# Performance work log

Hardware: AMD Instinct MI355X
Metric: run time of the kernel (lower is better)

The kernel has to match this reference:

```python
import jax, jax.numpy as jnp
import numpy as np

N, E = 65536, 524288
IN_DIM, HID_DIM, OUT_DIM = 1024, 512, 256


def setup_inputs() -> dict:
    key = jax.random.key(0)
    k1, k2, k3, k4, k5, k6 = jax.random.split(key, 6)
    h = jax.random.normal(k1, (N, IN_DIM), dtype=jnp.float32)
    src = jax.random.randint(k2, (E,), 0, N, dtype=jnp.int64)
    dst = jax.random.randint(k3, (E,), 0, N, dtype=jnp.int64)
    # Glorot-uniform weights as in DGL GraphConv
    lim1 = float(np.sqrt(6.0 / (IN_DIM + HID_DIM)))
    lim2 = float(np.sqrt(6.0 / (HID_DIM + OUT_DIM)))
    W1 = jax.random.uniform(k4, (IN_DIM, HID_DIM), jnp.float32, -lim1, lim1)
    W2 = jax.random.uniform(k5, (HID_DIM, OUT_DIM), jnp.float32, -lim2, lim2)
    b1 = jnp.zeros((HID_DIM,), jnp.float32)
    b2 = jnp.zeros((OUT_DIM,), jnp.float32)
    return {"h": h, "W1": W1, "b1": b1, "W2": W2, "b2": b2, "src": src, "dst": dst}


def _graph_conv(x, W, b, src, dst, inv_sqrt_dout, inv_sqrt_din):
    # DGL GraphConv, norm='both': D_in^{-1/2} A D_out^{-1/2} X W + b
    # Apply dense transform first (in_dim >= out_dim path in DGL) -- same math.
    x = x * inv_sqrt_dout[:, None]
    x = x @ W  # [N, out]
    agg = jax.ops.segment_sum(x[src], dst, num_segments=x.shape[0])  # scatter-add over edges
    return agg * inv_sqrt_din[:, None] + b


def reference(h, W1, b1, W2, b2, src, dst):
    n = h.shape[0]
    ones = jnp.ones((src.shape[0],), h.dtype)
    deg_out = jnp.maximum(jax.ops.segment_sum(ones, src, num_segments=n), 1.0)
    deg_in = jnp.maximum(jax.ops.segment_sum(ones, dst, num_segments=n), 1.0)
    inv_sqrt_dout = jax.lax.rsqrt(deg_out)
    inv_sqrt_din = jax.lax.rsqrt(deg_in)
    x = _graph_conv(h, W1, b1, src, dst, inv_sqrt_dout, inv_sqrt_din)
    x = jax.nn.elu(x)  # act; dropout p=0 -> identity
    out = _graph_conv(x, W2, b2, src, dst, inv_sqrt_dout, inv_sqrt_din)
    return out  # last_act = Identity
```

## Files before the change

### kernel.cpp

```cpp
#include <hip/hip_runtime.h>
#include <hip/hip_bf16.h>

#define IN_DIM 1024
#define HID 512
#define OUTD 256

typedef __attribute__((ext_vector_type(8))) short short8;
typedef __attribute__((ext_vector_type(4))) float f32x4;
typedef __attribute__((ext_vector_type(8))) unsigned short ushort8e;
typedef __attribute__((ext_vector_type(4))) unsigned short ushort4e;

template<int F> struct VecSel;
template<> struct VecSel<8> { using T = ushort8e; };
template<> struct VecSel<4> { using T = ushort4e; };


__device__ inline unsigned short f2bf(float f) {
    union { float f; unsigned u; } v; v.f = f;
    unsigned r = (v.u + 0x7FFF + ((v.u >> 16) & 1)) >> 16;
    return (unsigned short)r;
}

__device__ inline float bf2f(unsigned short u) {
    union { unsigned u; float f; } v; v.u = ((unsigned)u) << 16; return v.f;
}

__device__ inline void gload16(const void* g, void* l) {
    __builtin_amdgcn_global_load_lds(
        (const __attribute__((address_space(1))) void*)g,
        (__attribute__((address_space(3))) void*)l, 16, 0, 0);
}


__global__ void deg_kernel(const int* __restrict__ src, const int* __restrict__ dst,
                           int* __restrict__ dego, int* __restrict__ degi, int E) {
    int i = blockIdx.x * blockDim.x + threadIdx.x;
    if (i < E) {
        atomicAdd(&dego[src[i]], 1);
        atomicAdd(&degi[dst[i]], 1);
    }
}

__global__ void invsqrt_kernel(const int* __restrict__ dego, const int* __restrict__ degi,
                               float* __restrict__ iso, float* __restrict__ isi, int n) {
    int i = blockIdx.x * blockDim.x + threadIdx.x;
    if (i < n) {
        iso[i] = rsqrtf(fmaxf((float)dego[i], 1.0f));
        isi[i] = rsqrtf(fmaxf((float)degi[i], 1.0f));
    }
}


__global__ __launch_bounds__(256) void scan_block(const int* __restrict__ deg,
                                                  int* __restrict__ excl,
                                                  int* __restrict__ partials) {
    __shared__ int tmp[256];
    int tid = threadIdx.x;
    int i = blockIdx.x * 256 + tid;
    int v = deg[i];
    tmp[tid] = v;
    __syncthreads();
    #pragma unroll
    for (int off = 1; off < 256; off <<= 1) {
        int t = (tid >= off) ? tmp[tid - off] : 0;
        __syncthreads();
        tmp[tid] += t;
        __syncthreads();
    }
    excl[i] = tmp[tid] - v;
    if (tid == 255) partials[blockIdx.x] = tmp[255];
}

__global__ __launch_bounds__(256) void scan_partials(int* __restrict__ partials) {
    __shared__ int tmp[256];
    int tid = threadIdx.x;
    int v = partials[tid];
    tmp[tid] = v;
    __syncthreads();
    #pragma unroll
    for (int off = 1; off < 256; off <<= 1) {
        int t = (tid >= off) ? tmp[tid - off] : 0;
        __syncthreads();
        tmp[tid] += t;
        __syncthreads();
    }
    partials[tid] = tmp[tid] - v;
}

__global__ __launch_bounds__(256) void scan_add(const int* __restrict__ excl,
                                                const int* __restrict__ partials,
                                                const int* __restrict__ deg,
                                                int* __restrict__ row_start,
                                                int* __restrict__ cursor, int n) {
    int i = blockIdx.x * 256 + threadIdx.x;
    int v = excl[i] + partials[blockIdx.x];
    row_start[i] = v;
    cursor[i] = v;
    if (i == n - 1) row_start[n] = v + deg[i];
}

__global__ void csr_fill(const int* __restrict__ src, const int* __restrict__ dst,
                         int* __restrict__ cursor, int* __restrict__ eidx, int E) {
    int e = blockIdx.x * blockDim.x + threadIdx.x;
    if (e < E) {
        int pos = atomicAdd(&cursor[dst[e]], 1);
        eidx[pos] = src[e];
    }
}


__global__ void transpose_cvt(const float* __restrict__ W, unsigned short* __restrict__ Wt,
                              int K, int N) {
    int i = blockIdx.x * 256 + threadIdx.x;
    if (i < N * K) {
        int n = i / K, k = i - n * K;
        Wt[i] = f2bf(W[(size_t)k * N + n]);
    }
}


#define TM 128
#define TN 128
#define TK 32
#define NXCD 8

template<int AF32>
__global__ __launch_bounds__(256) void gemm_bf16_mfma(
    const void* __restrict__ Ap, const unsigned short* __restrict__ Bt,
    const float* __restrict__ rowscale, unsigned short* __restrict__ Cb,
    int M, int K, int Nc)
{
    __shared__ unsigned short As[TM][TK];
    __shared__ unsigned short Bs[TN][TK];

    const int tid  = threadIdx.x;
    const int lane = tid & 63;
    const int wave = tid >> 6;
    const int wr = wave >> 1, wc = wave & 1;
    const int lrow = lane & 15;
    const int lkg  = lane >> 4;

    const int nwg = gridDim.x;
    const int per = nwg / NXCD;
    const int lin = blockIdx.x;
    const int newlin = (lin % NXCD) * per + lin / NXCD;
    const int ncb = Nc / TN;
    const int m0 = (newlin / ncb) * TM;
    const int n0 = (newlin % ncb) * TN;

    const int s0 = wave * 64 + lane;
    const int s1 = s0 + 256;
    const int r0 = s0 >> 2, q0 = (s0 & 3) ^ ((s0 >> 3) & 3);
    const int r1 = s1 >> 2, q1 = (s1 & 3) ^ ((s1 >> 3) & 3);

    char* AsB = (char*)&As[0][0];
    char* BsB = (char*)&Bs[0][0];
    void* ldsA0 = AsB + wave * 1024;
    void* ldsA1 = AsB + 4096 + wave * 1024;
    void* ldsB0 = BsB + wave * 1024;
    void* ldsB1 = BsB + 4096 + wave * 1024;

    const int rA = tid >> 2;
    const int g  = tid & 3;
    const int jA = g ^ ((rA >> 1) & 3);
    float sc0 = 1.f, sc1 = 1.f;
    if (AF32) {
        sc0 = rowscale[m0 + rA];
        sc1 = rowscale[m0 + rA + 64];
    }
    const float* Af = (const float*)Ap;
    const unsigned short* Ab = (const unsigned short*)Ap;

    const int rslot = (lkg ^ ((lrow >> 1) & 3)) * 8;

    f32x4 acc[4][4] = {};

    const int nk = K / TK;
    for (int kt = 0; kt < nk; ++kt) {
        const int k0 = kt * TK;

        gload16(Bt + (size_t)(n0 + r0) * K + k0 + q0 * 8, ldsB0);
        gload16(Bt + (size_t)(n0 + r1) * K + k0 + q1 * 8, ldsB1);

        if (AF32) {
            const float* pa0 = Af + (size_t)(m0 + rA) * K + k0 + g * 8;
            const float* pa1 = Af + (size_t)(m0 + rA + 64) * K + k0 + g * 8;
            float4 u0 = *reinterpret_cast<const float4*>(pa0);
            float4 u1 = *reinterpret_cast<const float4*>(pa0 + 4);
            float4 w0 = *reinterpret_cast<const float4*>(pa1);
            float4 w1 = *reinterpret_cast<const float4*>(pa1 + 4);
            short8 pk0, pk1;
            pk0[0] = (short)f2bf(u0.x * sc0); pk0[1] = (short)f2bf(u0.y * sc0);
            pk0[2] = (short)f2bf(u0.z * sc0); pk0[3] = (short)f2bf(u0.w * sc0);
            pk0[4] = (short)f2bf(u1.x * sc0); pk0[5] = (short)f2bf(u1.y * sc0);
            pk0[6] = (short)f2bf(u1.z * sc0); pk0[7] = (short)f2bf(u1.w * sc0);
            pk1[0] = (short)f2bf(w0.x * sc1); pk1[1] = (short)f2bf(w0.y * sc1);
            pk1[2] = (short)f2bf(w0.z * sc1); pk1[3] = (short)f2bf(w0.w * sc1);
            pk1[4] = (short)f2bf(w1.x * sc1); pk1[5] = (short)f2bf(w1.y * sc1);
            pk1[6] = (short)f2bf(w1.z * sc1); pk1[7] = (short)f2bf(w1.w * sc1);
            *reinterpret_cast<short8*>(AsB + rA * 64 + jA * 16) = pk0;
            *reinterpret_cast<short8*>(AsB + (rA + 64) * 64 + jA * 16) = pk1;
        } else {
            gload16(Ab + (size_t)(m0 + r0) * K + k0 + q0 * 8, ldsA0);
            gload16(Ab + (size_t)(m0 + r1) * K + k0 + q1 * 8, ldsA1);
        }
        __syncthreads();

        short8 af[4], bfr[4];
        #pragma unroll
        for (int mi = 0; mi < 4; ++mi)
            af[mi] = *reinterpret_cast<const short8*>(&As[wr * 64 + mi * 16 + lrow][rslot]);
        #pragma unroll
        for (int ni = 0; ni < 4; ++ni)
            bfr[ni] = *reinterpret_cast<const short8*>(&Bs[wc * 64 + ni * 16 + lrow][rslot]);

        #pragma unroll
        for (int mi = 0; mi < 4; ++mi)
            #pragma unroll
            for (int ni = 0; ni < 4; ++ni)
                acc[mi][ni] = __builtin_amdgcn_mfma_f32_16x16x32_bf16(
                    af[mi], bfr[ni], acc[mi][ni], 0, 0, 0);

        __syncthreads();
    }

    #pragma unroll
    for (int mi = 0; mi < 4; ++mi)
        #pragma unroll
        for (int ni = 0; ni < 4; ++ni)
            #pragma unroll
            for (int r = 0; r < 4; ++r)
                Cb[(size_t)(m0 + wr * 64 + mi * 16 + lkg * 4 + r) * Nc
                   + (n0 + wc * 64 + ni * 16 + lrow)] = f2bf(acc[mi][ni][r]);
}


template<int DIM, bool LAYER1>
__global__ __launch_bounds__(256) void aggregate(
    const int* __restrict__ row_start, const int* __restrict__ eidx,
    const unsigned short* __restrict__ Xb, const float* __restrict__ isi,
    const float* __restrict__ iso, const float* __restrict__ bias,
    unsigned short* __restrict__ out_bf, float* __restrict__ out_f)
{
    constexpr int F = DIM / 64;
    using VecT = typename VecSel<F>::T;
    const int node = blockIdx.x * 4 + (threadIdx.x >> 6);
    const int lane = threadIdx.x & 63;

    const int beg = row_start[node];
    const int end = row_start[node + 1];
    const unsigned short* base = Xb + lane * F;

    float acc[F] = {};
    int e = beg;
    for (; e + 1 < end; e += 2) {
        int i0 = eidx[e], i1 = eidx[e + 1];
        VecT v0 = *reinterpret_cast<const VecT*>(base + (size_t)i0 * DIM);
        VecT v1 = *reinterpret_cast<const VecT*>(base + (size_t)i1 * DIM);
        #pragma unroll
        for (int f = 0; f < F; ++f) { acc[f] += bf2f(v0[f]); acc[f] += bf2f(v1[f]); }
    }
    if (e < end) {
        VecT v0 = *reinterpret_cast<const VecT*>(base + (size_t)eidx[e] * DIM);
        #pragma unroll
        for (int f = 0; f < F; ++f) acc[f] += bf2f(v0[f]);
    }

    const float si = isi[node];
    float bv[F];
    #pragma unroll
    for (int q = 0; q < F / 4; ++q)
        *reinterpret_cast<float4*>(&bv[q * 4]) =
            *reinterpret_cast<const float4*>(bias + lane * F + q * 4);

    if (LAYER1) {
        const float so = iso[node];
        short8 o;
        #pragma unroll
        for (int f = 0; f < F; ++f) {
            float v = acc[f] * si + bv[f];
            v = v > 0.f ? v : expm1f(v);
            o[f] = (short)f2bf(v * so);
        }
        *reinterpret_cast<short8*>(out_bf + (size_t)node * DIM + lane * F) = o;
    } else {
        #pragma unroll
        for (int q = 0; q < F / 4; ++q) {
            float4 v = make_float4(acc[q * 4 + 0] * si + bv[q * 4 + 0],
                                   acc[q * 4 + 1] * si + bv[q * 4 + 1],
                                   acc[q * 4 + 2] * si + bv[q * 4 + 2],
                                   acc[q * 4 + 3] * si + bv[q * 4 + 3]);
            *reinterpret_cast<float4*>(out_f + (size_t)node * DIM + lane * F + q * 4) = v;
        }
    }
}


extern "C" void kernel_launch(void* const* d_in, const int* in_sizes, int n_in,
                              void* d_out, int out_size, void* d_ws, size_t ws_size,
                              hipStream_t stream) {
    const float* h  = (const float*)d_in[0];
    const float* W1 = (const float*)d_in[1];
    const float* b1 = (const float*)d_in[2];
    const float* W2 = (const float*)d_in[3];
    const float* b2 = (const float*)d_in[4];
    const int*   src = (const int*)d_in[5];
    const int*   dst = (const int*)d_in[6];

    const int N = in_sizes[0] / IN_DIM;
    const int E = in_sizes[5];
    float* out = (float*)d_out;

    int* dego      = (int*)d_ws;
    int* degi      = dego + N;
    int* excl      = degi + N;
    int* partials  = excl + N;
    int* row_start = partials + 256;
    int* cursor    = row_start + N + 64;
    int* eidx      = cursor + N;
    float* iso     = (float*)(eidx + E);
    float* isi     = iso + N;
    unsigned short* W1t = (unsigned short*)(isi + N);
    unsigned short* W2t = W1t + (size_t)IN_DIM * HID;
    unsigned short* X1b = W2t + (size_t)HID * OUTD;
    unsigned short* X2b = X1b;
    unsigned short* R2h = X1b + (size_t)N * HID;

    hipMemsetAsync(dego, 0, sizeof(int) * (size_t)2 * N, stream);

    deg_kernel<<<(E + 255) / 256, 256, 0, stream>>>(src, dst, dego, degi, E);
    invsqrt_kernel<<<(N + 255) / 256, 256, 0, stream>>>(dego, degi, iso, isi, N);

    scan_block<<<N / 256, 256, 0, stream>>>(degi, excl, partials);
    scan_partials<<<1, 256, 0, stream>>>(partials);
    scan_add<<<N / 256, 256, 0, stream>>>(excl, partials, degi, row_start, cursor, N);
    csr_fill<<<(E + 255) / 256, 256, 0, stream>>>(src, dst, cursor, eidx, E);

    transpose_cvt<<<(IN_DIM * HID + 255) / 256, 256, 0, stream>>>(W1, W1t, IN_DIM, HID);
    transpose_cvt<<<(HID * OUTD + 255) / 256, 256, 0, stream>>>(W2, W2t, HID, OUTD);

    gemm_bf16_mfma<1><<<(N / TM) * (HID / TN), 256, 0, stream>>>(
        h, W1t, iso, X1b, N, IN_DIM, HID);
    aggregate<HID, true><<<N / 4, 256, 0, stream>>>(
        row_start, eidx, X1b, isi, iso, b1, R2h, nullptr);

    gemm_bf16_mfma<0><<<(N / TM) * (OUTD / TN), 256, 0, stream>>>(
        R2h, W2t, nullptr, X2b, N, HID, OUTD);
    aggregate<OUTD, false><<<N / 4, 256, 0, stream>>>(
        row_start, eidx, X2b, isi, iso, b2, nullptr, out);
}
```

Baseline: 407.2 us.

## Double-buffer LDS tiles in bf16 MFMA GEMM to overlap loads with compute

Doubles the A and B shared-memory tiles and prefetches the next K-slice, via async global-to-LDS loads or register staging for the fp32 A path, while MFMAs run on the current slice. One barrier per iteration is removed. The goal is to hide global load latency behind matrix math, at the cost of twice the LDS and extra registers for the staged fp32 A values, which may reduce occupancy.

New measurement: 404.7 us. No clear change (-0.6%).

```diff
diff --git a/kernel.cpp b/kernel.cpp
--- a/kernel.cpp
+++ b/kernel.cpp
@@ -124,14 +124,16 @@
 #define TK 32
 #define NXCD 8
 
+struct ARegs { float4 u0, u1, w0, w1; };
+
 template<int AF32>
 __global__ __launch_bounds__(256) void gemm_bf16_mfma(
     const void* __restrict__ Ap, const unsigned short* __restrict__ Bt,
     const float* __restrict__ rowscale, unsigned short* __restrict__ Cb,
     int M, int K, int Nc)
 {
-    __shared__ unsigned short As[TM][TK];
-    __shared__ unsigned short Bs[TN][TK];
+    __shared__ unsigned short As[2][TM][TK];
+    __shared__ unsigned short Bs[2][TN][TK];
 
     const int tid  = threadIdx.x;
     const int lane = tid & 63;
@@ -153,12 +155,8 @@
     const int r0 = s0 >> 2, q0 = (s0 & 3) ^ ((s0 >> 3) & 3);
     const int r1 = s1 >> 2, q1 = (s1 & 3) ^ ((s1 >> 3) & 3);
 
-    char* AsB = (char*)&As[0][0];
-    char* BsB = (char*)&Bs[0][0];
-    void* ldsA0 = AsB + wave * 1024;
-    void* ldsA1 = AsB + 4096 + wave * 1024;
-    void* ldsB0 = BsB + wave * 1024;
-    void* ldsB1 = BsB + 4096 + wave * 1024;
+    char* AsB = (char*)&As[0][0][0];
+    char* BsB = (char*)&Bs[0][0][0];
 
     const int rA = tid >> 2;
     const int g  = tid & 3;
@@ -173,46 +171,63 @@
 
     const int rslot = (lkg ^ ((lrow >> 1) & 3)) * 8;
 
+    auto stageB = [&](int kt, int buf) {
+        const int k0 = kt * TK;
+        gload16(Bt + (size_t)(n0 + r0) * K + k0 + q0 * 8, BsB + buf * 8192 + wave * 1024);
+        gload16(Bt + (size_t)(n0 + r1) * K + k0 + q1 * 8, BsB + buf * 8192 + 4096 + wave * 1024);
+    };
+    auto stageA_lds = [&](int kt, int buf) {
+        const int k0 = kt * TK;
+        gload16(Ab + (size_t)(m0 + r0) * K + k0 + q0 * 8, AsB + buf * 8192 + wave * 1024);
+        gload16(Ab + (size_t)(m0 + r1) * K + k0 + q1 * 8, AsB + buf * 8192 + 4096 + wave * 1024);
+    };
+    auto loadA = [&](int kt, ARegs& r) {
+        const float* pa0 = Af + (size_t)(m0 + rA) * K + kt * TK + g * 8;
+        const float* pa1 = pa0 + (size_t)64 * K;
+        r.u0 = *reinterpret_cast<const float4*>(pa0);
+        r.u1 = *reinterpret_cast<const float4*>(pa0 + 4);
+        r.w0 = *reinterpret_cast<const float4*>(pa1);
+        r.w1 = *reinterpret_cast<const float4*>(pa1 + 4);
+    };
+    auto writeA = [&](int buf, const ARegs& r) {
+        short8 pk0, pk1;
+        pk0[0] = (short)f2bf(r.u0.x * sc0); pk0[1] = (short)f2bf(r.u0.y * sc0);
+        pk0[2] = (short)f2bf(r.u0.z * sc0); pk0[3] = (short)f2bf(r.u0.w * sc0);
+        pk0[4] = (short)f2bf(r.u1.x * sc0); pk0[5] = (short)f2bf(r.u1.y * sc0);
+        pk0[6] = (short)f2bf(r.u1.z * sc0); pk0[7] = (short)f2bf(r.u1.w * sc0);
+        pk1[0] = (short)f2bf(r.w0.x * sc1); pk1[1] = (short)f2bf(r.w0.y * sc1);
+        pk1[2] = (short)f2bf(r.w0.z * sc1); pk1[3] = (short)f2bf(r.w0.w * sc1);
+        pk1[4] = (short)f2bf(r.w1.x * sc1); pk1[5] = (short)f2bf(r.w1.y * sc1);
+        pk1[6] = (short)f2bf(r.w1.z * sc1); pk1[7] = (short)f2bf(r.w1.w * sc1);
+        *reinterpret_cast<short8*>(AsB + buf * 8192 + rA * 64 + jA * 16) = pk0;
+        *reinterpret_cast<short8*>(AsB + buf * 8192 + (rA + 64) * 64 + jA * 16) = pk1;
+    };
+
     f32x4 acc[4][4] = {};
+    ARegs ar;
+
+    stageB(0, 0);
+    if (AF32) { loadA(0, ar); writeA(0, ar); }
+    else       stageA_lds(0, 0);
+    __syncthreads();
 
     const int nk = K / TK;
     for (int kt = 0; kt < nk; ++kt) {
-        const int k0 = kt * TK;
-
-        gload16(Bt + (size_t)(n0 + r0) * K + k0 + q0 * 8, ldsB0);
-        gload16(Bt + (size_t)(n0 + r1) * K + k0 + q1 * 8, ldsB1);
-
-        if (AF32) {
-            const float* pa0 = Af + (size_t)(m0 + rA) * K + k0 + g * 8;
-            const float* pa1 = Af + (size_t)(m0 + rA + 64) * K + k0 + g * 8;
-            float4 u0 = *reinterpret_cast<const float4*>(pa0);
-            float4 u1 = *reinterpret_cast<const float4*>(pa0 + 4);
-            float4 w0 = *reinterpret_cast<const float4*>(pa1);
-            float4 w1 = *reinterpret_cast<const float4*>(pa1 + 4);
-            short8 pk0, pk1;
-            pk0[0] = (short)f2bf(u0.x * sc0); pk0[1] = (short)f2bf(u0.y * sc0);
-            pk0[2] = (short)f2bf(u0.z * sc0); pk0[3] = (short)f2bf(u0.w * sc0);
-            pk0[4] = (short)f2bf(u1.x * sc0); pk0[5] = (short)f2bf(u1.y * sc0);
-            pk0[6] = (short)f2bf(u1.z * sc0); pk0[7] = (short)f2bf(u1.w * sc0);
-            pk1[0] = (short)f2bf(w0.x * sc1); pk1[1] = (short)f2bf(w0.y * sc1);
-            pk1[2] = (short)f2bf(w0.z * sc1); pk1[3] = (short)f2bf(w0.w * sc1);
-            pk1[4] = (short)f2bf(w1.x * sc1); pk1[5] = (short)f2bf(w1.y * sc1);
-            pk1[6] = (short)f2bf(w1.z * sc1); pk1[7] = (short)f2bf(w1.w * sc1);
-            *reinterpret_cast<short8*>(AsB + rA * 64 + jA * 16) = pk0;
-            *reinterpret_cast<short8*>(AsB + (rA + 64) * 64 + jA * 16) = pk1;
-        } else {
-            gload16(Ab + (size_t)(m0 + r0) * K + k0 + q0 * 8, ldsA0);
-            gload16(Ab + (size_t)(m0 + r1) * K + k0 + q1 * 8, ldsA1);
+        const int cur = kt & 1, nxt = cur ^ 1;
+
+        if (kt + 1 < nk) {
+            stageB(kt + 1, nxt);
+            if (AF32) loadA(kt + 1, ar);
+            else      stageA_lds(kt + 1, nxt);
         }
-        __syncthreads();
 
         short8 af[4], bfr[4];
         #pragma unroll
         for (int mi = 0; mi < 4; ++mi)
-            af[mi] = *reinterpret_cast<const short8*>(&As[wr * 64 + mi * 16 + lrow][rslot]);
+            af[mi] = *reinterpret_cast<const short8*>(&As[cur][wr * 64 + mi * 16 + lrow][rslot]);
         #pragma unroll
         for (int ni = 0; ni < 4; ++ni)
-            bfr[ni] = *reinterpret_cast<const short8*>(&Bs[wc * 64 + ni * 16 + lrow][rslot]);
+            bfr[ni] = *reinterpret_cast<const short8*>(&Bs[cur][wc * 64 + ni * 16 + lrow][rslot]);
 
         #pragma unroll
         for (int mi = 0; mi < 4; ++mi)
@@ -220,6 +235,8 @@
             for (int ni = 0; ni < 4; ++ni)
                 acc[mi][ni] = __builtin_amdgcn_mfma_f32_16x16x32_bf16(
                     af[mi], bfr[ni], acc[mi][ni], 0, 0, 0);
+
+        if (AF32 && kt + 1 < nk) writeA(nxt, ar);
 
         __syncthreads();
     }
```
